# Optimization experiments

Hardware: AMD Instinct MI355X
Metric: run time of the kernel (lower is better)

Reference implementation:

```python
import jax, jax.numpy as jnp
import numpy as np

D_IN = 1024
D_OUT = 1024
H = 16


def setup_inputs() -> dict:
    key = jax.random.key(0)
    ks = jax.random.split(key, 11)
    B, Tq, Tk = 2, 2048, 2048
    s = 1.0 / np.sqrt(D_IN)
    return {
        "q": jax.random.normal(ks[0], (B, Tq, D_IN), jnp.float32),
        "k": jax.random.normal(ks[1], (B, Tk, D_IN), jnp.float32),
        "v": jax.random.normal(ks[2], (B, Tk, D_IN), jnp.float32),
        "Wq": jax.random.uniform(ks[3], (D_IN, D_OUT), jnp.float32, -s, s),
        "bq": jax.random.uniform(ks[4], (D_OUT,), jnp.float32, -s, s),
        "Wk": jax.random.uniform(ks[5], (D_IN, D_OUT), jnp.float32, -s, s),
        "bk": jax.random.uniform(ks[6], (D_OUT,), jnp.float32, -s, s),
        "Wv": jax.random.uniform(ks[7], (D_IN, D_OUT), jnp.float32, -s, s),
        "bv": jax.random.uniform(ks[8], (D_OUT,), jnp.float32, -s, s),
        "Wo": jax.random.uniform(ks[9], (D_OUT, D_OUT), jnp.float32, -s, s),
        "bo": jax.random.uniform(ks[10], (D_OUT,), jnp.float32, -s, s),
    }


def reference(q, k, v, Wq, bq, Wk, bk, Wv, bv, Wo, bo):
    B, Tq, _ = q.shape
    Tk = k.shape[1]
    hd = D_OUT // H
    # QKV projections, split heads -> [B, H, T, hd]
    qh = (q @ Wq + bq).reshape(B, Tq, H, hd).transpose(0, 2, 1, 3)
    kh = (k @ Wk + bk).reshape(B, Tk, H, hd).transpose(0, 2, 1, 3)
    vh = (v @ Wv + bv).reshape(B, Tk, H, hd).transpose(0, 2, 1, 3)
    # scaled dot-product attention (scale uses key dim = head_dim)
    scores = jnp.einsum("bhqd,bhkd->bhqk", qh, kh) / jnp.sqrt(jnp.float32(hd))
    attn = jax.nn.softmax(scores, axis=-1)
    x = jnp.einsum("bhqk,bhkd->bhqd", attn, vh)
    x = x.transpose(0, 2, 1, 3).reshape(B, Tq, D_OUT)
    return x @ Wo + bo
```

## Files before the change

### kernel.cpp

```cpp
#include <hip/hip_runtime.h>
#include <hip/hip_bf16.h>

typedef __attribute__((ext_vector_type(8))) short short8;
typedef __attribute__((ext_vector_type(4))) short short4v;
typedef __attribute__((ext_vector_type(4))) float f32x4;

__device__ __forceinline__ unsigned short f2bf(float f) {
    __hip_bfloat16 h = __float2bfloat16(f);
    unsigned short u;
    __builtin_memcpy(&u, &h, 2);
    return u;
}
__device__ __forceinline__ short4v pack4bf(float a, float b, float c, float d) {
    union { __hip_bfloat162 h[2]; short4v s; } r;
    r.h[0] = __float22bfloat162_rn(make_float2(a, b));
    r.h[1] = __float22bfloat162_rn(make_float2(c, d));
    return r.s;
}

#define GLD16(gp, lp) __builtin_amdgcn_global_load_lds( \
    (const __attribute__((address_space(1))) void*)(gp), \
    (__attribute__((address_space(3))) void*)(lp), 16, 0, 0)

__global__ __launch_bounds__(256) void prep(
    const float* __restrict__ q, const float* __restrict__ k, const float* __restrict__ v,
    unsigned short* __restrict__ qb, unsigned short* __restrict__ kb, unsigned short* __restrict__ vb,
    const float* __restrict__ W0, const float* __restrict__ W1,
    const float* __restrict__ W2, const float* __restrict__ W3,
    unsigned short* __restrict__ T0, unsigned short* __restrict__ T1,
    unsigned short* __restrict__ T2, unsigned short* __restrict__ T3)
{
    __shared__ unsigned short Ts[64 * 72];
    int bx = blockIdx.x;
    if (bx < 6144) {
        const float* src; unsigned short* dst;
        switch (bx >> 11) { case 0: src = q; dst = qb; break;
                            case 1: src = k; dst = kb; break;
                            default: src = v; dst = vb; break; }
        size_t i = ((size_t)(bx & 2047) * 256 + threadIdx.x) * 8;
        float4 x0 = *(const float4*)&src[i];
        float4 x1 = *(const float4*)&src[i + 4];
        union { unsigned short s[8]; uint4 u; } p;
        p.s[0] = f2bf(x0.x); p.s[1] = f2bf(x0.y); p.s[2] = f2bf(x0.z); p.s[3] = f2bf(x0.w);
        p.s[4] = f2bf(x1.x); p.s[5] = f2bf(x1.y); p.s[6] = f2bf(x1.z); p.s[7] = f2bf(x1.w);
        *(uint4*)&dst[i] = p.u;
        return;
    }
    int w = bx - 6144;
    int z = w >> 8, rem = w & 255;
    int kx = rem >> 4, ny = rem & 15;
    const float* W;
    unsigned short* T;
    switch (z) {
        case 0: W = W0; T = T0; break;
        case 1: W = W1; T = T1; break;
        case 2: W = W2; T = T2; break;
        default: W = W3; T = T3; break;
    }
    int tid = threadIdx.x;
    int c = tid & 7, r = tid >> 3;
    int k0 = kx * 64, n0 = ny * 64;
    for (int i = 0; i < 64; i += 32) {
        const float* src = &W[(size_t)(k0 + r + i) * 1024 + n0 + c * 8];
        float4 x0 = *(const float4*)src;
        float4 x1 = *(const float4*)(src + 4);
        unsigned short* d = &Ts[(r + i) * 72 + c * 8];
        d[0] = f2bf(x0.x); d[1] = f2bf(x0.y); d[2] = f2bf(x0.z); d[3] = f2bf(x0.w);
        d[4] = f2bf(x1.x); d[5] = f2bf(x1.y); d[6] = f2bf(x1.z); d[7] = f2bf(x1.w);
    }
    __syncthreads();
    for (int i = 0; i < 64; i += 32) {
        union { unsigned short s[8]; uint4 v; } u;
        for (int j = 0; j < 8; j++) u.s[j] = Ts[(c * 8 + j) * 72 + (r + i)];
        *(uint4*)&T[(size_t)(n0 + r + i) * 1024 + k0 + c * 8] = u.v;
    }
}

__device__ __forceinline__ void gemm_core(
    const unsigned short* __restrict__ A, const unsigned short* __restrict__ BT,
    const float* __restrict__ bias, void* __restrict__ outv,
    int mode, float scale)
{
    const int K = 1024;
    __shared__ unsigned short As[128 * 32];
    __shared__ unsigned short Bs[128 * 32];
    int tid = threadIdx.x;
    int m0 = blockIdx.x * 128, n0 = blockIdx.y * 128;
    int lane = tid & 63, wave = tid >> 6;
    int lm = lane & 15, quad = lane >> 4;
    int wm = (wave >> 1) * 64, wn = (wave & 1) * 64;

    int lrow = lane >> 2;
    int scol = ((lane & 3) ^ ((lane >> 3) & 3)) * 8;
    const unsigned short* Ag = A + (size_t)(m0 + wave * 32 + lrow) * K + scol;
    const unsigned short* Bg = BT + (size_t)(n0 + wave * 32 + lrow) * K + scol;
    unsigned short* AsW0 = &As[(wave * 32) * 32];
    unsigned short* AsW1 = &As[(wave * 32 + 16) * 32];
    unsigned short* BsW0 = &Bs[(wave * 32) * 32];
    unsigned short* BsW1 = &Bs[(wave * 32 + 16) * 32];

    int rpos = (quad ^ ((lm >> 1) & 3)) * 8;

    f32x4 acc[4][4];
    for (int i = 0; i < 4; i++)
        for (int j = 0; j < 4; j++)
            for (int r = 0; r < 4; r++) acc[i][j][r] = 0.0f;

    for (int kb = 0; kb < K; kb += 32) {
        GLD16(Ag, AsW0);
        GLD16(Ag + 16 * K, AsW1);
        GLD16(Bg, BsW0);
        GLD16(Bg + 16 * K, BsW1);
        Ag += 32; Bg += 32;
        __syncthreads();
        short8 a[4], b[4];
        for (int i = 0; i < 4; i++)
            a[i] = *(const short8*)&As[(wm + i * 16 + lm) * 32 + rpos];
        for (int j = 0; j < 4; j++)
            b[j] = *(const short8*)&Bs[(wn + j * 16 + lm) * 32 + rpos];
        for (int i = 0; i < 4; i++)
            for (int j = 0; j < 4; j++)
                acc[i][j] = __builtin_amdgcn_mfma_f32_16x16x32_bf16(a[i], b[j], acc[i][j], 0, 0, 0);
        __syncthreads();
    }

    for (int j = 0; j < 4; j++) {
        int col = n0 + wn + j * 16 + lm;
        float bv = bias[col];
        for (int i = 0; i < 4; i++) {
            int rowb = m0 + wm + i * 16 + quad * 4;
            if (mode == 0) {
                float* out32 = (float*)outv;
                for (int r = 0; r < 4; r++)
                    out32[(size_t)(rowb + r) * 1024 + col] = (acc[i][j][r] + bv) * scale;
            } else if (mode == 1) {
                unsigned short* out16 = (unsigned short*)outv;
                int h = col >> 6, d = col & 63;
                int bb = rowb >> 11, t = rowb & 2047;
                size_t base = (((size_t)(bb * 16 + h)) * 2048 + t) * 64 + d;
                for (int r = 0; r < 4; r++)
                    out16[base + (size_t)r * 64] = f2bf((acc[i][j][r] + bv) * scale);
            } else {
                unsigned short* out16 = (unsigned short*)outv;
                int h = col >> 6, d = col & 63;
                int bb = rowb >> 11, t = rowb & 2047;
                ushort4 pk;
                pk.x = f2bf((acc[i][j][0] + bv) * scale);
                pk.y = f2bf((acc[i][j][1] + bv) * scale);
                pk.z = f2bf((acc[i][j][2] + bv) * scale);
                pk.w = f2bf((acc[i][j][3] + bv) * scale);
                *(ushort4*)&out16[(((size_t)(bb * 16 + h)) * 64 + d) * 2048 + t] = pk;
            }
        }
    }
}

__global__ __launch_bounds__(256) void qkv_gemm(
    const unsigned short* __restrict__ qbf, const unsigned short* __restrict__ kbf,
    const unsigned short* __restrict__ vbf,
    const unsigned short* __restrict__ WqT, const unsigned short* __restrict__ WkT,
    const unsigned short* __restrict__ WvT,
    const float* __restrict__ bq, const float* __restrict__ bk, const float* __restrict__ bv,
    unsigned short* __restrict__ Qh, unsigned short* __restrict__ Kh,
    unsigned short* __restrict__ VhT)
{
    switch (blockIdx.z) {
        case 0:  gemm_core(qbf, WqT, bq, Qh,  1, 0.18033688011f); break;
        case 1:  gemm_core(kbf, WkT, bk, Kh,  1, 1.0f);           break;
        default: gemm_core(vbf, WvT, bv, VhT, 2, 1.0f);           break;
    }
}

__global__ __launch_bounds__(256) void out_gemm(
    const unsigned short* __restrict__ X, const unsigned short* __restrict__ WoT,
    const float* __restrict__ bo, float* __restrict__ out)
{
    gemm_core(X, WoT, bo, out, 0, 1.0f);
}

__global__ __launch_bounds__(256) void attn_kernel(
    const unsigned short* __restrict__ Qh, const unsigned short* __restrict__ Kh,
    const unsigned short* __restrict__ VhT, unsigned short* __restrict__ X)
{
    __shared__ unsigned short Ks[4][64 * 64];
    __shared__ unsigned short Vt[4][64 * 64];

    int tid = threadIdx.x;
    int qblk = blockIdx.x & 15, bh = blockIdx.x >> 4;
    int b = bh >> 4, h = bh & 15;
    int lane = tid & 63, wave = tid >> 6;
    int lm = lane & 15, quad = lane >> 4;

    const unsigned short* Kbase = Kh + (size_t)bh * 2048 * 64;
    const unsigned short* Vbase = VhT + (size_t)bh * 64 * 2048;

    int srow = wave * 8 + (lane >> 3);
    int schk = ((lane & 7) ^ ((lane >> 3) & 7)) * 8;
    int swz  = lm & 7;

    const char* ks0 = (const char*)&Ks[0][0] + lm * 128 + ((quad ^ swz) * 16);
    const char* ks1 = (const char*)&Ks[0][0] + lm * 128 + (((quad + 4) ^ swz) * 16);
    int qh2 = quad >> 1, wo = (quad & 1) * 8;
    const char* vt0 = (const char*)&Vt[0][0] + lm * 128 + (((0 + qh2) ^ swz) * 16) + wo;
    const char* vt1 = (const char*)&Vt[0][0] + lm * 128 + (((2 + qh2) ^ swz) * 16) + wo;
    const char* vt2 = (const char*)&Vt[0][0] + lm * 128 + (((4 + qh2) ^ swz) * 16) + wo;
    const char* vt3 = (const char*)&Vt[0][0] + lm * 128 + (((6 + qh2) ^ swz) * 16) + wo;

    const unsigned short* Kg = Kbase + (size_t)srow * 64 + schk;
    const unsigned short* Vg = Vbase + (size_t)srow * 2048 + schk;

    int qrow = qblk * 128 + wave * 32 + lm;
    const unsigned short* qptr = Qh + ((size_t)bh * 2048 + qrow) * 64;
    short8 qfa0 = *(const short8*)&qptr[quad * 8];
    short8 qfa1 = *(const short8*)&qptr[32 + quad * 8];
    short8 qfb0 = *(const short8*)&qptr[16 * 64 + quad * 8];
    short8 qfb1 = *(const short8*)&qptr[16 * 64 + 32 + quad * 8];
    asm volatile("s_waitcnt vmcnt(0)" ::: "memory");

    f32x4 oA[4], oB[4];
    for (int n = 0; n < 4; n++)
        for (int r = 0; r < 4; r++) { oA[n][r] = 0.0f; oB[n][r] = 0.0f; }
    float lA = 0.0f, lB = 0.0f;
    f32x4 zf;
    zf[0] = zf[1] = zf[2] = zf[3] = 0.0f;

#define STAGE(BUF) do { \
        GLD16(Kg,             &Ks[BUF][(wave * 8) * 64]); \
        GLD16(Kg + 32 * 64,   &Ks[BUF][(32 + wave * 8) * 64]); \
        GLD16(Vg,             &Vt[BUF][(wave * 8) * 64]); \
        GLD16(Vg + 32 * 2048, &Vt[BUF][(32 + wave * 8) * 64]); \
        Kg += 64 * 64; Vg += 64; } while (0)

#define PHASE(WAITN) do { \
        asm volatile("s_waitcnt vmcnt(" #WAITN ")" ::: "memory"); \
        __builtin_amdgcn_s_barrier(); \
        asm volatile("" ::: "memory"); \
        __builtin_amdgcn_sched_barrier(0); } while (0)

#define QKPV(CUR) do { \
        short4v pa[4], pb[4]; \
        _Pragma("unroll") \
        for (int t = 0; t < 4; t++) { \
            short8 ka0 = *(const short8*)(ks0 + (CUR) * 8192 + t * 2048); \
            short8 ka1 = *(const short8*)(ks1 + (CUR) * 8192 + t * 2048); \
            f32x4 za = __builtin_amdgcn_mfma_f32_16x16x32_bf16(ka0, qfa0, zf, 0, 0, 0); \
            za = __builtin_amdgcn_mfma_f32_16x16x32_bf16(ka1, qfa1, za, 0, 0, 0); \
            f32x4 zb = __builtin_amdgcn_mfma_f32_16x16x32_bf16(ka0, qfb0, zf, 0, 0, 0); \
            zb = __builtin_amdgcn_mfma_f32_16x16x32_bf16(ka1, qfb1, zb, 0, 0, 0); \
            float a0 = __builtin_amdgcn_exp2f(za[0]); \
            float a1 = __builtin_amdgcn_exp2f(za[1]); \
            float a2 = __builtin_amdgcn_exp2f(za[2]); \
            float a3 = __builtin_amdgcn_exp2f(za[3]); \
            lA += (a0 + a1) + (a2 + a3); \
            pa[t] = pack4bf(a0, a1, a2, a3); \
            float b0 = __builtin_amdgcn_exp2f(zb[0]); \
            float b1 = __builtin_amdgcn_exp2f(zb[1]); \
            float b2 = __builtin_amdgcn_exp2f(zb[2]); \
            float b3 = __builtin_amdgcn_exp2f(zb[3]); \
            lB += (b0 + b1) + (b2 + b3); \
            pb[t] = pack4bf(b0, b1, b2, b3); \
        } \
        _Pragma("unroll") \
        for (int n = 0; n < 4; n++) { \
            short4v v0 = *(const short4v*)(vt0 + (CUR) * 8192 + n * 2048); \
            short4v v1 = *(const short4v*)(vt1 + (CUR) * 8192 + n * 2048); \
            short4v v2 = *(const short4v*)(vt2 + (CUR) * 8192 + n * 2048); \
            short4v v3 = *(const short4v*)(vt3 + (CUR) * 8192 + n * 2048); \
            oA[n] = __builtin_amdgcn_mfma_f32_16x16x16bf16_1k(pa[0], v0, oA[n], 0, 0, 0); \
            oB[n] = __builtin_amdgcn_mfma_f32_16x16x16bf16_1k(pb[0], v0, oB[n], 0, 0, 0); \
            oA[n] = __builtin_amdgcn_mfma_f32_16x16x16bf16_1k(pa[1], v1, oA[n], 0, 0, 0); \
            oB[n] = __builtin_amdgcn_mfma_f32_16x16x16bf16_1k(pb[1], v1, oB[n], 0, 0, 0); \
            oA[n] = __builtin_amdgcn_mfma_f32_16x16x16bf16_1k(pa[2], v2, oA[n], 0, 0, 0); \
            oB[n] = __builtin_amdgcn_mfma_f32_16x16x16bf16_1k(pb[2], v2, oB[n], 0, 0, 0); \
            oA[n] = __builtin_amdgcn_mfma_f32_16x16x16bf16_1k(pa[3], v3, oA[n], 0, 0, 0); \
            oB[n] = __builtin_amdgcn_mfma_f32_16x16x16bf16_1k(pb[3], v3, oB[n], 0, 0, 0); \
        } } while (0)

    STAGE(0); STAGE(1); STAGE(2);

    for (int u = 0; u < 7; u++) {
        PHASE(8); STAGE(3); QKPV(0);
        PHASE(8); STAGE(0); QKPV(1);
        PHASE(8); STAGE(1); QKPV(2);
        PHASE(8); STAGE(2); QKPV(3);
    }
    PHASE(8); STAGE(3); QKPV(0);
    PHASE(8); QKPV(1);
    PHASE(4); QKPV(2);
    PHASE(0); QKPV(3);

#undef STAGE
#undef PHASE
#undef QKPV

    lA += __shfl_xor(lA, 16);
    lA += __shfl_xor(lA, 32);
    lB += __shfl_xor(lB, 16);
    lB += __shfl_xor(lB, 32);
    float invA = 1.0f / lA;
    float invB = 1.0f / lB;

    for (int r = 0; r < 4; r++) {
        int src = (lane & 48) | (quad * 4 + r);
        float invAr = __shfl(invA, src);
        float invBr = __shfl(invB, src);
        int rowA = qblk * 128 + wave * 32 + quad * 4 + r;
        for (int n = 0; n < 4; n++) {
            X[((size_t)b * 2048 + rowA) * 1024 + h * 64 + n * 16 + lm] = f2bf(oA[n][r] * invAr);
            X[((size_t)b * 2048 + rowA + 16) * 1024 + h * 64 + n * 16 + lm] = f2bf(oB[n][r] * invBr);
        }
    }
}

extern "C" void kernel_launch(void* const* d_in, const int* in_sizes, int n_in,
                              void* d_out, int out_size, void* d_ws, size_t ws_size,
                              hipStream_t stream)
{
    const float* q  = (const float*)d_in[0];
    const float* k  = (const float*)d_in[1];
    const float* v  = (const float*)d_in[2];
    const float* Wq = (const float*)d_in[3];
    const float* bq = (const float*)d_in[4];
    const float* Wk = (const float*)d_in[5];
    const float* bk = (const float*)d_in[6];
    const float* Wv = (const float*)d_in[7];
    const float* bv = (const float*)d_in[8];
    const float* Wo = (const float*)d_in[9];
    const float* bo = (const float*)d_in[10];

    unsigned short* ws  = (unsigned short*)d_ws;
    const unsigned int M1 = 1u << 20;
    unsigned short* WqT = ws;
    unsigned short* WkT = ws + M1;
    unsigned short* WvT = ws + 2 * M1;
    unsigned short* WoT = ws + 3 * M1;
    unsigned short* qbf = ws + 4 * M1;
    unsigned short* kbf = ws + 8 * M1;
    unsigned short* vbf = ws + 12 * M1;
    unsigned short* Qh  = ws + 16 * M1;
    unsigned short* Kh  = ws + 4 * M1;
    unsigned short* VhT = ws + 8 * M1;
    unsigned short* X   = ws + 12 * M1;

    prep<<<dim3(7168), 256, 0, stream>>>(q, k, v, qbf, kbf, vbf,
                                         Wq, Wk, Wv, Wo, WqT, WkT, WvT, WoT);
    qkv_gemm<<<dim3(32, 8, 3), 256, 0, stream>>>(qbf, kbf, vbf, WqT, WkT, WvT,
                                                 bq, bk, bv, Qh, Kh, VhT);
    attn_kernel<<<dim3(512), 256, 0, stream>>>(Qh, Kh, VhT, X);
    out_gemm<<<dim3(32, 8), 256, 0, stream>>>(X, WoT, bo, (float*)d_out);
}
```

Before: 220.3 us.

## Double GEMM K-step to 64 with 8-way swizzle and narrower out-projection tiles

The shared GEMM core now stages 64-wide K slices per iteration with an XOR swizzle over 8 chunks, which halves the number of barrier pairs and global-to-LDS rounds per tile. The out-projection gets its own kernel with 128x64 tiles, giving 512 blocks instead of 256 so more of the CUs have work, and launch bounds are added to control occupancy. The price is twice the LDS per block and more registers live across the unrolled inner loop.

```diff
diff --git a/kernel.cpp b/kernel.cpp
--- a/kernel.cpp
+++ b/kernel.cpp
@@ -76,51 +76,55 @@
     }
 }
 
-__device__ __forceinline__ void gemm_core(
+__device__ __forceinline__ void gemm128_core(
     const unsigned short* __restrict__ A, const unsigned short* __restrict__ BT,
-    const float* __restrict__ bias, void* __restrict__ outv,
+    const float* __restrict__ bias, unsigned short* __restrict__ out16,
     int mode, float scale)
 {
     const int K = 1024;
-    __shared__ unsigned short As[128 * 32];
-    __shared__ unsigned short Bs[128 * 32];
+    __shared__ unsigned short As[128 * 64];
+    __shared__ unsigned short Bs[128 * 64];
     int tid = threadIdx.x;
     int m0 = blockIdx.x * 128, n0 = blockIdx.y * 128;
     int lane = tid & 63, wave = tid >> 6;
     int lm = lane & 15, quad = lane >> 4;
     int wm = (wave >> 1) * 64, wn = (wave & 1) * 64;
 
-    int lrow = lane >> 2;
-    int scol = ((lane & 3) ^ ((lane >> 3) & 3)) * 8;
+    int lrow = lane >> 3;
+    int scol = ((lane & 7) ^ lrow) * 8;
     const unsigned short* Ag = A + (size_t)(m0 + wave * 32 + lrow) * K + scol;
     const unsigned short* Bg = BT + (size_t)(n0 + wave * 32 + lrow) * K + scol;
-    unsigned short* AsW0 = &As[(wave * 32) * 32];
-    unsigned short* AsW1 = &As[(wave * 32 + 16) * 32];
-    unsigned short* BsW0 = &Bs[(wave * 32) * 32];
-    unsigned short* BsW1 = &Bs[(wave * 32 + 16) * 32];
-
-    int rpos = (quad ^ ((lm >> 1) & 3)) * 8;
+    unsigned short* AsW = &As[(wave * 32) * 64];
+    unsigned short* BsW = &Bs[(wave * 32) * 64];
 
     f32x4 acc[4][4];
     for (int i = 0; i < 4; i++)
         for (int j = 0; j < 4; j++)
             for (int r = 0; r < 4; r++) acc[i][j][r] = 0.0f;
 
-    for (int kb = 0; kb < K; kb += 32) {
-        GLD16(Ag, AsW0);
-        GLD16(Ag + 16 * K, AsW1);
-        GLD16(Bg, BsW0);
-        GLD16(Bg + 16 * K, BsW1);
-        Ag += 32; Bg += 32;
+    for (int kb = 0; kb < K; kb += 64) {
+        GLD16(Ag,          AsW);
+        GLD16(Ag +  8 * K, AsW +  8 * 64);
+        GLD16(Ag + 16 * K, AsW + 16 * 64);
+        GLD16(Ag + 24 * K, AsW + 24 * 64);
+        GLD16(Bg,          BsW);
+        GLD16(Bg +  8 * K, BsW +  8 * 64);
+        GLD16(Bg + 16 * K, BsW + 16 * 64);
+        GLD16(Bg + 24 * K, BsW + 24 * 64);
+        Ag += 64; Bg += 64;
         __syncthreads();
-        short8 a[4], b[4];
-        for (int i = 0; i < 4; i++)
-            a[i] = *(const short8*)&As[(wm + i * 16 + lm) * 32 + rpos];
-        for (int j = 0; j < 4; j++)
-            b[j] = *(const short8*)&Bs[(wn + j * 16 + lm) * 32 + rpos];
-        for (int i = 0; i < 4; i++)
+#pragma unroll
+        for (int kk = 0; kk < 2; kk++) {
+            int rp = ((kk * 4 + quad) ^ (lm & 7)) * 8;
+            short8 a[4], b[4];
+            for (int i = 0; i < 4; i++)
+                a[i] = *(const short8*)&As[(wm + i * 16 + lm) * 64 + rp];
             for (int j = 0; j < 4; j++)
-                acc[i][j] = __builtin_amdgcn_mfma_f32_16x16x32_bf16(a[i], b[j], acc[i][j], 0, 0, 0);
+                b[j] = *(const short8*)&Bs[(wn + j * 16 + lm) * 64 + rp];
+            for (int i = 0; i < 4; i++)
+                for (int j = 0; j < 4; j++)
+                    acc[i][j] = __builtin_amdgcn_mfma_f32_16x16x32_bf16(a[i], b[j], acc[i][j], 0, 0, 0);
+        }
         __syncthreads();
     }
 
@@ -129,21 +133,13 @@
         float bv = bias[col];
         for (int i = 0; i < 4; i++) {
             int rowb = m0 + wm + i * 16 + quad * 4;
-            if (mode == 0) {
-                float* out32 = (float*)outv;
-                for (int r = 0; r < 4; r++)
-                    out32[(size_t)(rowb + r) * 1024 + col] = (acc[i][j][r] + bv) * scale;
-            } else if (mode == 1) {
-                unsigned short* out16 = (unsigned short*)outv;
-                int h = col >> 6, d = col & 63;
-                int bb = rowb >> 11, t = rowb & 2047;
+            int h = col >> 6, d = col & 63;
+            int bb = rowb >> 11, t = rowb & 2047;
+            if (mode == 1) {
                 size_t base = (((size_t)(bb * 16 + h)) * 2048 + t) * 64 + d;
                 for (int r = 0; r < 4; r++)
                     out16[base + (size_t)r * 64] = f2bf((acc[i][j][r] + bv) * scale);
             } else {
-                unsigned short* out16 = (unsigned short*)outv;
-                int h = col >> 6, d = col & 63;
-                int bb = rowb >> 11, t = rowb & 2047;
                 ushort4 pk;
                 pk.x = f2bf((acc[i][j][0] + bv) * scale);
                 pk.y = f2bf((acc[i][j][1] + bv) * scale);
@@ -155,7 +151,7 @@
     }
 }
 
-__global__ __launch_bounds__(256) void qkv_gemm(
+__global__ __launch_bounds__(256, 3) void qkv_gemm(
     const unsigned short* __restrict__ qbf, const unsigned short* __restrict__ kbf,
     const unsigned short* __restrict__ vbf,
     const unsigned short* __restrict__ WqT, const unsigned short* __restrict__ WkT,
@@ -165,17 +161,70 @@
     unsigned short* __restrict__ VhT)
 {
     switch (blockIdx.z) {
-        case 0:  gemm_core(qbf, WqT, bq, Qh,  1, 0.18033688011f); break;
-        case 1:  gemm_core(kbf, WkT, bk, Kh,  1, 1.0f);           break;
-        default: gemm_core(vbf, WvT, bv, VhT, 2, 1.0f);           break;
-    }
-}
-
-__global__ __launch_bounds__(256) void out_gemm(
-    const unsigned short* __restrict__ X, const unsigned short* __restrict__ WoT,
-    const float* __restrict__ bo, float* __restrict__ out)
-{
-    gemm_core(X, WoT, bo, out, 0, 1.0f);
+        case 0:  gemm128_core(qbf, WqT, bq, Qh,  1, 0.18033688011f); break;
+        case 1:  gemm128_core(kbf, WkT, bk, Kh,  1, 1.0f);           break;
+        default: gemm128_core(vbf, WvT, bv, VhT, 2, 1.0f);           break;
+    }
+}
+
+__global__ __launch_bounds__(256, 2) void out_gemm(
+    const unsigned short* __restrict__ A, const unsigned short* __restrict__ BT,
+    const float* __restrict__ bias, float* __restrict__ out)
+{
+    const int K = 1024;
+    __shared__ unsigned short As[128 * 64];
+    __shared__ unsigned short Bs[64 * 64];
+    int tid = threadIdx.x;
+    int m0 = blockIdx.x * 128, n0 = blockIdx.y * 64;
+    int lane = tid & 63, wave = tid >> 6;
+    int lm = lane & 15, quad = lane >> 4;
+    int wm = wave * 32;
+
+    int lrow = lane >> 3;
+    int scol = ((lane & 7) ^ lrow) * 8;
+    const unsigned short* Ag = A + (size_t)(m0 + wave * 32 + lrow) * K + scol;
+    const unsigned short* Bg = BT + (size_t)(n0 + wave * 16 + lrow) * K + scol;
+    unsigned short* AsW = &As[(wave * 32) * 64];
+    unsigned short* BsW = &Bs[(wave * 16) * 64];
+
+    f32x4 acc[2][4];
+    for (int i = 0; i < 2; i++)
+        for (int j = 0; j < 4; j++)
+            for (int r = 0; r < 4; r++) acc[i][j][r] = 0.0f;
+
+    for (int kb = 0; kb < K; kb += 64) {
+        GLD16(Ag,          AsW);
+        GLD16(Ag +  8 * K, AsW +  8 * 64);
+        GLD16(Ag + 16 * K, AsW + 16 * 64);
+        GLD16(Ag + 24 * K, AsW + 24 * 64);
+        GLD16(Bg,          BsW);
+        GLD16(Bg +  8 * K, BsW +  8 * 64);
+        Ag += 64; Bg += 64;
+        __syncthreads();
+#pragma unroll
+        for (int kk = 0; kk < 2; kk++) {
+            int rp = ((kk * 4 + quad) ^ (lm & 7)) * 8;
+            short8 a[2], b[4];
+            for (int i = 0; i < 2; i++)
+                a[i] = *(const short8*)&As[(wm + i * 16 + lm) * 64 + rp];
+            for (int j = 0; j < 4; j++)
+                b[j] = *(const short8*)&Bs[(j * 16 + lm) * 64 + rp];
+            for (int i = 0; i < 2; i++)
+                for (int j = 0; j < 4; j++)
+                    acc[i][j] = __builtin_amdgcn_mfma_f32_16x16x32_bf16(a[i], b[j], acc[i][j], 0, 0, 0);
+        }
+        __syncthreads();
+    }
+
+    for (int j = 0; j < 4; j++) {
+        int col = n0 + j * 16 + lm;
+        float bv = bias[col];
+        for (int i = 0; i < 2; i++) {
+            int rowb = m0 + wm + i * 16 + quad * 4;
+            for (int r = 0; r < 4; r++)
+                out[(size_t)(rowb + r) * 1024 + col] = acc[i][j][r] + bv;
+        }
+    }
 }
 
 __global__ __launch_bounds__(256) void attn_kernel(
@@ -347,5 +396,5 @@
     qkv_gemm<<<dim3(32, 8, 3), 256, 0, stream>>>(qbf, kbf, vbf, WqT, WkT, WvT,
                                                  bq, bk, bv, Qh, Kh, VhT);
     attn_kernel<<<dim3(512), 256, 0, stream>>>(Qh, Kh, VhT, X);
-    out_gemm<<<dim3(32, 8), 256, 0, stream>>>(X, WoT, bo, (float*)d_out);
-}
+    out_gemm<<<dim3(32, 16), 256, 0, stream>>>(X, WoT, bo, (float*)d_out);
+}
```

Result: no change. 224.1 us (+1.7%).
